# Kernel tuning notes

Hardware: AMD Instinct MI355X
Metric: run time of the kernel (lower is better)

## Reference

```python
import jax, jax.numpy as jnp
import numpy as np

EMBED_DIM = 1024
NUM_HEADS = 16
HEAD_DIM = EMBED_DIM // NUM_HEADS


def setup_inputs() -> dict:
    key = jax.random.key(0)
    k_x, k_wqkv, k_bqkv, k_wo, k_bo = jax.random.split(key, 5)
    b, n = 2, 2048
    scale_in = 1.0 / np.sqrt(EMBED_DIM)
    return {
        "x": jax.random.normal(k_x, (b, n, EMBED_DIM), dtype=jnp.float32),
        "W_qkv": jax.random.normal(k_wqkv, (EMBED_DIM, 3 * EMBED_DIM), dtype=jnp.float32) * scale_in,
        "b_qkv": jnp.zeros((3 * EMBED_DIM,), dtype=jnp.float32),
        "W_out": jax.random.normal(k_wo, (EMBED_DIM, EMBED_DIM), dtype=jnp.float32) * scale_in,
        "b_out": jnp.zeros((EMBED_DIM,), dtype=jnp.float32),
    }


def _rope_rotate(t, cos, sin):
    # t: [b, h, n, hd]; cos/sin: [1, 1, n, hd//2]
    t1, t2 = jnp.split(t, 2, axis=-1)
    return jnp.concatenate([cos * t1 - sin * t2, sin * t1 + cos * t2], axis=-1)


def reference(x, W_qkv, b_qkv, W_out, b_out):
    b, n, d = x.shape
    h, hd = NUM_HEADS, HEAD_DIM

    qkv = x @ W_qkv + b_qkv                      # [b, n, 3d]
    q, k, v = jnp.split(qkv, 3, axis=-1)
    q, k, v = [t.reshape(b, n, h, hd).transpose(0, 2, 1, 3) for t in (q, k, v)]

    # RoPE tables
    hd2 = hd // 2
    theta = 10000.0 ** (-2.0 * jnp.arange(hd2, dtype=jnp.float32) / hd)
    freqs = jnp.arange(n, dtype=jnp.float32)[:, None] * theta[None, :]  # [n, hd2]
    cos = jnp.cos(freqs)[None, None]
    sin = jnp.sin(freqs)[None, None]
    q = _rope_rotate(q, cos, sin)
    k = _rope_rotate(k, cos, sin)

    scores = jnp.einsum('bhqd,bhkd->bhqk', q, k) / jnp.sqrt(jnp.float32(hd))
    attn = jax.nn.softmax(scores, axis=-1)       # [b, h, n, n]
    out = jnp.einsum('bhqk,bhkd->bhqd', attn, v)
    out = out.transpose(0, 2, 1, 3).reshape(b, n, d)
    return out @ W_out + b_out
```

## Files before the change

kernel.cpp:

```cpp
#include <hip/hip_runtime.h>
#include <hip/hip_bf16.h>
#include <math.h>

#define EMBED 1024
#define NHEAD 16
#define HD 64
#define BATCH 2
#define SEQ 2048
#define MTOT (BATCH * SEQ)
#define QKVN (3 * EMBED)

typedef __attribute__((ext_vector_type(8))) short short8;
typedef __attribute__((ext_vector_type(4))) float f32x4;

typedef __attribute__((address_space(1))) const unsigned int GUI;
typedef __attribute__((address_space(3))) unsigned int LUI;

__device__ __forceinline__ void gload_lds16(const void* src, void* dst) {
  __builtin_amdgcn_global_load_lds((GUI*)src, (LUI*)dst, 16, 0, 0);
}

__device__ __forceinline__ unsigned short f2bf(float f) {
  unsigned u = __builtin_bit_cast(unsigned, f);
  u += 0x7fffu + ((u >> 16) & 1u);
  return (unsigned short)(u >> 16);
}

__device__ __forceinline__ unsigned cvt_pk_bf16(float lo, float hi) {
  unsigned r;
  asm("v_cvt_pk_bf16_f32 %0, %1, %2" : "=v"(r) : "v"(lo), "v"(hi));
  return r;
}

#define QSCALE 0.1803368801111191f


__global__ __launch_bounds__(256) void k_cvt(const float* __restrict__ in,
                                             unsigned short* __restrict__ out, int n4) {
  int i = blockIdx.x * 256 + threadIdx.x;
  if (i >= n4) return;
  float4 v = reinterpret_cast<const float4*>(in)[i];
  ushort4 o;
  o.x = f2bf(v.x); o.y = f2bf(v.y); o.z = f2bf(v.z); o.w = f2bf(v.w);
  reinterpret_cast<ushort4*>(out)[i] = o;
}

__global__ __launch_bounds__(256) void k_transpose_cvt(const float* __restrict__ W,
                                                       unsigned short* __restrict__ WT,
                                                       int K, int Ncols) {
  __shared__ float tile[32][33];
  int n0 = blockIdx.x * 32, k0 = blockIdx.y * 32;
  int tc = threadIdx.x & 31, tr = threadIdx.x >> 5;
  for (int i = 0; i < 4; i++) {
    int r = tr + i * 8;
    tile[r][tc] = W[(size_t)(k0 + r) * Ncols + n0 + tc];
  }
  __syncthreads();
  for (int i = 0; i < 4; i++) {
    int r = tr + i * 8;
    WT[(size_t)(n0 + r) * K + k0 + tc] = f2bf(tile[tc][r]);
  }
}

__global__ __launch_bounds__(256) void k_rope_tables(float* __restrict__ cosT,
                                                     float* __restrict__ sinT) {
  int idx = blockIdx.x * 256 + threadIdx.x;
  if (idx >= SEQ * 32) return;
  int pos = idx >> 5, i = idx & 31;
  float theta = __expf((float)i * -0.28782313662425575f);
  float f = (float)pos * theta;
  cosT[idx] = cosf(f);
  sinT[idx] = sinf(f);
}

__device__ __forceinline__ void gemm_mainloop(const unsigned short* __restrict__ A,
                                              const unsigned short* __restrict__ Bt,
                                              unsigned short* Al, unsigned short* Bl,
                                              size_t m0, size_t n0,
                                              int tid, int l15, int g, int wm, int wn,
                                              f32x4 acc[4][4]) {
  const int w = tid >> 6;
  const int lane = tid & 63;
  const int srow = lane >> 3, slot = lane & 7;
  for (int k0 = 0; k0 < 1024; k0 += 64) {
    __syncthreads();
    for (int it = 0; it < 4; it++) {
      const int r = w * 32 + it * 8 + srow;
      const int sc = (slot ^ (r & 7)) * 8;
      gload_lds16(A + (m0 + r) * 1024 + k0 + sc, &Al[(w * 32 + it * 8) * 64]);
      gload_lds16(Bt + (n0 + r) * 1024 + k0 + sc, &Bl[(w * 32 + it * 8) * 64]);
    }
    __syncthreads();
    for (int kk = 0; kk < 2; kk++) {
      short8 fa[4], fb[4];
      const int xr = ((kk * 4 + g) ^ (l15 & 7)) * 8;
      for (int i = 0; i < 4; i++)
        fa[i] = *reinterpret_cast<const short8*>(&Al[(wm * 64 + i * 16 + l15) * 64 + xr]);
      for (int j = 0; j < 4; j++)
        fb[j] = *reinterpret_cast<const short8*>(&Bl[(wn * 64 + j * 16 + l15) * 64 + xr]);
      for (int i = 0; i < 4; i++)
        for (int j = 0; j < 4; j++)
          acc[i][j] = __builtin_amdgcn_mfma_f32_16x16x32_bf16(fa[i], fb[j], acc[i][j], 0, 0, 0);
    }
  }
}

__global__ __launch_bounds__(256) void k_qkv_gemm(const unsigned short* __restrict__ A,
                                                  const unsigned short* __restrict__ Bt,
                                                  const float* __restrict__ bias,
                                                  const float* __restrict__ cosT,
                                                  const float* __restrict__ sinT,
                                                  unsigned short* __restrict__ Qb,
                                                  unsigned short* __restrict__ Kb,
                                                  unsigned short* __restrict__ Vtg) {
  __shared__ alignas(16) unsigned short Al[128 * 64];
  __shared__ alignas(16) unsigned short Bl[128 * 64];
  const int tid = threadIdx.x;
  const int lane = tid & 63, l15 = lane & 15, g = lane >> 4;
  const int wid = tid >> 6, wm = wid >> 1, wn = wid & 1;
  const size_t m0 = (size_t)blockIdx.y * 128;
  const size_t n0 = (size_t)blockIdx.x * 128;
  f32x4 acc[4][4] = {};
  gemm_mainloop(A, Bt, Al, Bl, m0, n0, tid, l15, g, wm, wn, acc);

  const int cbase = (int)n0 + wn * 64;
  const int sec = cbase >> 10;
  const int head = (cbase & 1023) >> 6;
  float bia[4];
  for (int j = 0; j < 4; j++) bia[j] = bias[cbase + j * 16 + l15];
  const size_t mw = m0 + wm * 64;

  if (sec == 2) {
    for (int i = 0; i < 4; i++) {
      size_t mbase = mw + i * 16 + g * 4;
      int bb = (int)(mbase >> 11), pos0 = (int)(mbase & 2047);
      int k0 = pos0 & 63;
      int col = (pos0 & ~63) | (k0 & 32) | (((k0 >> 2) & 3) << 3) | (((k0 >> 4) & 1) << 2);
      size_t hb = (size_t)(bb * NHEAD + head) * HD;
      for (int j = 0; j < 4; j++) {
        int d = j * 16 + l15;
        uint2 pk;
        pk.x = cvt_pk_bf16(acc[i][j][0] + bia[j], acc[i][j][1] + bia[j]);
        pk.y = cvt_pk_bf16(acc[i][j][2] + bia[j], acc[i][j][3] + bia[j]);
        *reinterpret_cast<uint2*>(Vtg + (hb + d) * SEQ + col) = pk;
      }
    }
  } else {
    unsigned short* dst = sec ? Kb : Qb;
    const float qs = sec ? 1.0f : QSCALE;
    for (int i = 0; i < 4; i++)
      for (int r = 0; r < 4; r++) {
        size_t m = mw + i * 16 + g * 4 + r;
        int bb = (int)(m >> 11), pos = (int)(m & 2047);
        size_t base = ((size_t)(bb * NHEAD + head) * SEQ + pos) * HD;
        const float* cr = cosT + pos * 32;
        const float* sr = sinT + pos * 32;
        for (int pl = 0; pl < 2; pl++) {
          int ii = pl * 16 + l15;
          float c = cr[ii], s = sr[ii];
          float lo = acc[i][pl][r] + bia[pl];
          float hi = acc[i][pl + 2][r] + bia[pl + 2];
          dst[base + ii]      = f2bf((c * lo - s * hi) * qs);
          dst[base + 32 + ii] = f2bf((s * lo + c * hi) * qs);
        }
      }
  }
}

__global__ __launch_bounds__(256) void k_out_gemm(const unsigned short* __restrict__ A,
                                                  const unsigned short* __restrict__ Bt,
                                                  const float* __restrict__ bias,
                                                  float* __restrict__ out) {
  __shared__ alignas(16) unsigned short Al[128 * 64];
  __shared__ alignas(16) unsigned short Bl[64 * 64];
  const int tid = threadIdx.x;
  const int lane = tid & 63, l15 = lane & 15, g = lane >> 4;
  const int wid = tid >> 6, wm = wid >> 1, wn = wid & 1;
  const int w = wid;
  const int srow = lane >> 3, slot = lane & 7;
  const size_t m0 = (size_t)blockIdx.y * 128;
  const size_t n0 = (size_t)blockIdx.x * 64;
  f32x4 acc[4][2] = {};

  for (int k0 = 0; k0 < 1024; k0 += 64) {
    __syncthreads();
    for (int it = 0; it < 4; it++) {
      const int r = w * 32 + it * 8 + srow;
      const int sc = (slot ^ (r & 7)) * 8;
      gload_lds16(A + (m0 + r) * 1024 + k0 + sc, &Al[(w * 32 + it * 8) * 64]);
    }
    for (int it = 0; it < 2; it++) {
      const int r = w * 16 + it * 8 + srow;
      const int sc = (slot ^ (r & 7)) * 8;
      gload_lds16(Bt + (n0 + r) * 1024 + k0 + sc, &Bl[(w * 16 + it * 8) * 64]);
    }
    __syncthreads();
    for (int kk = 0; kk < 2; kk++) {
      short8 fa[4], fb[2];
      const int xr = ((kk * 4 + g) ^ (l15 & 7)) * 8;
      for (int i = 0; i < 4; i++)
        fa[i] = *reinterpret_cast<const short8*>(&Al[(wm * 64 + i * 16 + l15) * 64 + xr]);
      for (int j = 0; j < 2; j++)
        fb[j] = *reinterpret_cast<const short8*>(&Bl[(wn * 32 + j * 16 + l15) * 64 + xr]);
      for (int i = 0; i < 4; i++)
        for (int j = 0; j < 2; j++)
          acc[i][j] = __builtin_amdgcn_mfma_f32_16x16x32_bf16(fa[i], fb[j], acc[i][j], 0, 0, 0);
    }
  }

  const int cbase = (int)n0 + wn * 32;
  const size_t mw = m0 + wm * 64;
  for (int i = 0; i < 4; i++)
    for (int r = 0; r < 4; r++) {
      size_t m = mw + i * 16 + g * 4 + r;
      for (int j = 0; j < 2; j++) {
        int col = cbase + j * 16 + l15;
        out[m * EMBED + col] = acc[i][j][r] + bias[col];
      }
    }
}

__global__ __launch_bounds__(256) void k_attn(const unsigned short* __restrict__ Q,
                                              const unsigned short* __restrict__ Kg,
                                              const unsigned short* __restrict__ Vtg,
                                              float* __restrict__ Opart,
                                              float* __restrict__ lpart) {
  __shared__ alignas(16) unsigned short Kt[64 * 64];
  __shared__ alignas(16) unsigned short Vt[64 * 64];
  const int tid = threadIdx.x, w = tid >> 6, lane = tid & 63;
  const int l15 = lane & 15, g = lane >> 4;
  const int srow = lane >> 3, slot = lane & 7;

  const int n = blockIdx.x;
  const int xcd = n & 7, m = n >> 3;
  const int qb = m & 15, z = m >> 4;
  const int sp = z & 1, bh = (z >> 1) * 8 + xcd;

  const unsigned short* Qp = Q + (size_t)bh * SEQ * HD;
  const unsigned short* Kp = Kg + (size_t)bh * SEQ * HD;
  const unsigned short* Vp = Vtg + (size_t)bh * HD * SEQ;
  const int q0 = qb * 128 + w * 32;

  short8 aq[2][2];
#pragma unroll
  for (int u = 0; u < 2; u++)
#pragma unroll
    for (int kk = 0; kk < 2; kk++)
      aq[u][kk] = *reinterpret_cast<const short8*>(
          Qp + (size_t)(q0 + u * 16 + l15) * HD + kk * 32 + g * 8);

  const int sr16 = w * 16 + srow;
  const int sc0 = (slot ^ (sr16 & 7)) * 8;

  f32x4 o[2][4] = {};
  float lrow[2] = {0.f, 0.f};

  for (int t = sp * 16; t < sp * 16 + 16; t++) {
    const int kb = t * 64;
    __syncthreads();
    gload_lds16(Kp + (size_t)(kb + sr16) * HD + sc0, &Kt[(w * 16) * 64]);
    gload_lds16(Vp + (size_t)sr16 * SEQ + kb + sc0, &Vt[(w * 16) * 64]);
    gload_lds16(Kp + (size_t)(kb + sr16 + 8) * HD + sc0, &Kt[(w * 16 + 8) * 64]);
    gload_lds16(Vp + (size_t)(sr16 + 8) * SEQ + kb + sc0, &Vt[(w * 16 + 8) * 64]);
    __syncthreads();

    f32x4 s[2][4] = {};
#pragma unroll
    for (int kk = 0; kk < 2; kk++) {
      const int xr = ((kk * 4 + g) ^ (l15 & 7)) * 8;
#pragma unroll
      for (int c = 0; c < 4; c++) {
        short8 ak = *reinterpret_cast<const short8*>(&Kt[(c * 16 + l15) * 64 + xr]);
        s[0][c] = __builtin_amdgcn_mfma_f32_16x16x32_bf16(ak, aq[0][kk], s[0][c], 0, 0, 0);
        s[1][c] = __builtin_amdgcn_mfma_f32_16x16x32_bf16(ak, aq[1][kk], s[1][c], 0, 0, 0);
      }
    }

    unsigned wpk[2][8];
#pragma unroll
    for (int u = 0; u < 2; u++) {
      float rs = 0.f;
#pragma unroll
      for (int c = 0; c < 4; c++) {
        float p0 = __builtin_exp2f(s[u][c][0]);
        float p1 = __builtin_exp2f(s[u][c][1]);
        float p2 = __builtin_exp2f(s[u][c][2]);
        float p3 = __builtin_exp2f(s[u][c][3]);
        rs += (p0 + p1) + (p2 + p3);
        wpk[u][2 * c]     = cvt_pk_bf16(p0, p1);
        wpk[u][2 * c + 1] = cvt_pk_bf16(p2, p3);
      }
      lrow[u] += rs;
    }

#pragma unroll
    for (int kk = 0; kk < 2; kk++) {
      const int xr = ((kk * 4 + g) ^ (l15 & 7)) * 8;
      short8 pb0 = __builtin_bit_cast(short8,
          uint4{wpk[0][4 * kk], wpk[0][4 * kk + 1], wpk[0][4 * kk + 2], wpk[0][4 * kk + 3]});
      short8 pb1 = __builtin_bit_cast(short8,
          uint4{wpk[1][4 * kk], wpk[1][4 * kk + 1], wpk[1][4 * kk + 2], wpk[1][4 * kk + 3]});
#pragma unroll
      for (int c2 = 0; c2 < 4; c2++) {
        short8 av = *reinterpret_cast<const short8*>(&Vt[(c2 * 16 + l15) * 64 + xr]);
        o[0][c2] = __builtin_amdgcn_mfma_f32_16x16x32_bf16(av, pb0, o[0][c2], 0, 0, 0);
        o[1][c2] = __builtin_amdgcn_mfma_f32_16x16x32_bf16(av, pb1, o[1][c2], 0, 0, 0);
      }
    }
  }

  const size_t ob = (size_t)(sp * 32 + bh) * HD * SEQ;
#pragma unroll
  for (int u = 0; u < 2; u++) {
    float l = lrow[u];
    l += __shfl_xor(l, 16, 64);
    l += __shfl_xor(l, 32, 64);
    const int pos = q0 + u * 16 + l15;
    if (g == 0) lpart[(size_t)(sp * 32 + bh) * SEQ + pos] = l;
#pragma unroll
    for (int c2 = 0; c2 < 4; c2++)
#pragma unroll
      for (int r = 0; r < 4; r++)
        Opart[ob + (size_t)(c2 * 16 + g * 4 + r) * SEQ + pos] = o[u][c2][r];
  }
}

__global__ __launch_bounds__(256) void k_merge(const float* __restrict__ Op,
                                               const float* __restrict__ lp,
                                               unsigned short* __restrict__ AO) {
  __shared__ float T[64][65];
  __shared__ float Ls[64];
  const int tid = threadIdx.x;
  const int bh = blockIdx.x & 31, pt = blockIdx.x >> 5;
  const int p0 = pt * 64;
  const size_t b0 = (size_t)bh * HD * SEQ;
  const size_t b1 = (size_t)(32 + bh) * HD * SEQ;
  const int pc = tid & 63, dr = tid >> 6;
#pragma unroll
  for (int pass = 0; pass < 16; pass++) {
    const int d = pass * 4 + dr;
    T[d][pc] = Op[b0 + (size_t)d * SEQ + p0 + pc] + Op[b1 + (size_t)d * SEQ + p0 + pc];
  }
  if (tid < 64)
    Ls[tid] = lp[(size_t)bh * SEQ + p0 + tid] + lp[(size_t)(32 + bh) * SEQ + p0 + tid];
  __syncthreads();
  const int pos = tid >> 2, dc = (tid & 3) * 16;
  const float inv = 1.f / Ls[pos];
  const int bb = bh >> 4, h = bh & 15;
  unsigned short* dst = AO + ((size_t)bb * SEQ + p0 + pos) * EMBED + h * HD + dc;
  unsigned pk[8];
#pragma unroll
  for (int i = 0; i < 8; i++)
    pk[i] = cvt_pk_bf16(T[dc + 2 * i][pos] * inv, T[dc + 2 * i + 1][pos] * inv);
  *reinterpret_cast<uint4*>(dst) = uint4{pk[0], pk[1], pk[2], pk[3]};
  *reinterpret_cast<uint4*>(dst + 8) = uint4{pk[4], pk[5], pk[6], pk[7]};
}

extern "C" void kernel_launch(void* const* d_in, const int* in_sizes, int n_in,
                              void* d_out, int out_size, void* d_ws, size_t ws_size,
                              hipStream_t stream) {
  const float* x    = (const float*)d_in[0];
  const float* Wqkv = (const float*)d_in[1];
  const float* bqkv = (const float*)d_in[2];
  const float* Wout = (const float*)d_in[3];
  const float* bout = (const float*)d_in[4];
  float* out = (float*)d_out;

  char* ws = (char*)d_ws;
  size_t off = 0;
  auto carve = [&](size_t bytes) {
    char* p = ws + off;
    off += (bytes + 255) & ~(size_t)255;
    return p;
  };
  float* cosT           = (float*)carve((size_t)SEQ * 32 * 4);
  float* sinT           = (float*)carve((size_t)SEQ * 32 * 4);
  unsigned short* Xb    = (unsigned short*)carve((size_t)MTOT * EMBED * 2);
  unsigned short* WqkvT = (unsigned short*)carve((size_t)QKVN * EMBED * 2);
  unsigned short* WoT   = (unsigned short*)carve((size_t)EMBED * EMBED * 2);
  unsigned short* Qb    = (unsigned short*)carve((size_t)MTOT * EMBED * 2);
  unsigned short* Kb    = (unsigned short*)carve((size_t)MTOT * EMBED * 2);
  unsigned short* Vtg   = (unsigned short*)carve((size_t)MTOT * EMBED * 2);
  unsigned short* AO    = (unsigned short*)carve((size_t)MTOT * EMBED * 2);
  float* Opart          = (float*)carve((size_t)2 * 32 * HD * SEQ * 4);
  float* lpart          = (float*)carve((size_t)2 * 32 * SEQ * 4);

  k_cvt<<<(MTOT * EMBED / 4 + 255) / 256, 256, 0, stream>>>(x, Xb, MTOT * EMBED / 4);
  k_transpose_cvt<<<dim3(QKVN / 32, EMBED / 32), 256, 0, stream>>>(Wqkv, WqkvT, EMBED, QKVN);
  k_transpose_cvt<<<dim3(EMBED / 32, EMBED / 32), 256, 0, stream>>>(Wout, WoT, EMBED, EMBED);
  k_rope_tables<<<(SEQ * 32) / 256, 256, 0, stream>>>(cosT, sinT);

  k_qkv_gemm<<<dim3(QKVN / 128, MTOT / 128), 256, 0, stream>>>(Xb, WqkvT, bqkv, cosT, sinT, Qb, Kb, Vtg);
  k_attn<<<dim3(1024), 256, 0, stream>>>(Qb, Kb, Vtg, Opart, lpart);
  k_merge<<<dim3(1024), 256, 0, stream>>>(Opart, lpart, AO);
  k_out_gemm<<<dim3(EMBED / 64, MTOT / 128), 256, 0, stream>>>(AO, WoT, bout, out);
}
```

Baseline: 149.4 us.

## Double-buffer K/V tiles in attention kernel to overlap loads with MFMA

Splits the K and V shared-memory tiles into two buffers. The next tile's global-to-LDS loads are issued before computing on the current one, with a partial vmcnt wait and raw barriers replacing the load-then-sync pattern. This is meant to hide global memory latency behind the QK/PV matrix work. LDS usage doubles, which could reduce occupancy.

New measurement: 146.7 us. About the same (-1.8%).

```diff
diff --git a/kernel.cpp b/kernel.cpp
--- a/kernel.cpp
+++ b/kernel.cpp
@@ -225,8 +225,8 @@
                                               const unsigned short* __restrict__ Vtg,
                                               float* __restrict__ Opart,
                                               float* __restrict__ lpart) {
-  __shared__ alignas(16) unsigned short Kt[64 * 64];
-  __shared__ alignas(16) unsigned short Vt[64 * 64];
+  __shared__ alignas(16) unsigned short Kt[2][64 * 64];
+  __shared__ alignas(16) unsigned short Vt[2][64 * 64];
   const int tid = threadIdx.x, w = tid >> 6, lane = tid & 63;
   const int l15 = lane & 15, g = lane >> 4;
   const int srow = lane >> 3, slot = lane & 7;
@@ -251,63 +251,79 @@
 
   const int sr16 = w * 16 + srow;
   const int sc0 = (slot ^ (sr16 & 7)) * 8;
+  const int kb0 = sp * 1024;
 
   f32x4 o[2][4] = {};
   float lrow[2] = {0.f, 0.f};
 
-  for (int t = sp * 16; t < sp * 16 + 16; t++) {
-    const int kb = t * 64;
-    __syncthreads();
-    gload_lds16(Kp + (size_t)(kb + sr16) * HD + sc0, &Kt[(w * 16) * 64]);
-    gload_lds16(Vp + (size_t)sr16 * SEQ + kb + sc0, &Vt[(w * 16) * 64]);
-    gload_lds16(Kp + (size_t)(kb + sr16 + 8) * HD + sc0, &Kt[(w * 16 + 8) * 64]);
-    gload_lds16(Vp + (size_t)(sr16 + 8) * SEQ + kb + sc0, &Vt[(w * 16 + 8) * 64]);
-    __syncthreads();
-
-    f32x4 s[2][4] = {};
-#pragma unroll
-    for (int kk = 0; kk < 2; kk++) {
-      const int xr = ((kk * 4 + g) ^ (l15 & 7)) * 8;
-#pragma unroll
-      for (int c = 0; c < 4; c++) {
-        short8 ak = *reinterpret_cast<const short8*>(&Kt[(c * 16 + l15) * 64 + xr]);
-        s[0][c] = __builtin_amdgcn_mfma_f32_16x16x32_bf16(ak, aq[0][kk], s[0][c], 0, 0, 0);
-        s[1][c] = __builtin_amdgcn_mfma_f32_16x16x32_bf16(ak, aq[1][kk], s[1][c], 0, 0, 0);
-      }
-    }
-
-    unsigned wpk[2][8];
-#pragma unroll
-    for (int u = 0; u < 2; u++) {
-      float rs = 0.f;
-#pragma unroll
-      for (int c = 0; c < 4; c++) {
-        float p0 = __builtin_exp2f(s[u][c][0]);
-        float p1 = __builtin_exp2f(s[u][c][1]);
-        float p2 = __builtin_exp2f(s[u][c][2]);
-        float p3 = __builtin_exp2f(s[u][c][3]);
-        rs += (p0 + p1) + (p2 + p3);
-        wpk[u][2 * c]     = cvt_pk_bf16(p0, p1);
-        wpk[u][2 * c + 1] = cvt_pk_bf16(p2, p3);
-      }
-      lrow[u] += rs;
-    }
-
-#pragma unroll
-    for (int kk = 0; kk < 2; kk++) {
-      const int xr = ((kk * 4 + g) ^ (l15 & 7)) * 8;
-      short8 pb0 = __builtin_bit_cast(short8,
-          uint4{wpk[0][4 * kk], wpk[0][4 * kk + 1], wpk[0][4 * kk + 2], wpk[0][4 * kk + 3]});
-      short8 pb1 = __builtin_bit_cast(short8,
-          uint4{wpk[1][4 * kk], wpk[1][4 * kk + 1], wpk[1][4 * kk + 2], wpk[1][4 * kk + 3]});
-#pragma unroll
-      for (int c2 = 0; c2 < 4; c2++) {
-        short8 av = *reinterpret_cast<const short8*>(&Vt[(c2 * 16 + l15) * 64 + xr]);
-        o[0][c2] = __builtin_amdgcn_mfma_f32_16x16x32_bf16(av, pb0, o[0][c2], 0, 0, 0);
-        o[1][c2] = __builtin_amdgcn_mfma_f32_16x16x32_bf16(av, pb1, o[1][c2], 0, 0, 0);
-      }
-    }
-  }
+#define STAGE(tt, b)                                                             \
+  do {                                                                           \
+    const int kb_ = kb0 + (tt) * 64;                                             \
+    gload_lds16(Kp + (size_t)(kb_ + sr16) * HD + sc0, &Kt[b][(w * 16) * 64]);    \
+    gload_lds16(Vp + (size_t)sr16 * SEQ + kb_ + sc0, &Vt[b][(w * 16) * 64]);     \
+    gload_lds16(Kp + (size_t)(kb_ + sr16 + 8) * HD + sc0,                        \
+                &Kt[b][(w * 16 + 8) * 64]);                                      \
+    gload_lds16(Vp + (size_t)(sr16 + 8) * SEQ + kb_ + sc0,                       \
+                &Vt[b][(w * 16 + 8) * 64]);                                      \
+  } while (0)
+
+#define COMPUTE(cur)                                                             \
+  do {                                                                           \
+    const unsigned short* Ktc = Kt[cur];                                         \
+    const unsigned short* Vtc = Vt[cur];                                         \
+    f32x4 s[2][4] = {};                                                          \
+    _Pragma("unroll") for (int kk = 0; kk < 2; kk++) {                           \
+      const int xr = ((kk * 4 + g) ^ (l15 & 7)) * 8;                             \
+      _Pragma("unroll") for (int c = 0; c < 4; c++) {                            \
+        short8 ak = *reinterpret_cast<const short8*>(&Ktc[(c * 16 + l15) * 64 + xr]); \
+        s[0][c] = __builtin_amdgcn_mfma_f32_16x16x32_bf16(ak, aq[0][kk], s[0][c], 0, 0, 0); \
+        s[1][c] = __builtin_amdgcn_mfma_f32_16x16x32_bf16(ak, aq[1][kk], s[1][c], 0, 0, 0); \
+      }                                                                          \
+    }                                                                            \
+    unsigned wpk[2][8];                                                          \
+    _Pragma("unroll") for (int u = 0; u < 2; u++) {                              \
+      float rs = 0.f;                                                            \
+      _Pragma("unroll") for (int c = 0; c < 4; c++) {                            \
+        float p0 = __builtin_exp2f(s[u][c][0]);                                  \
+        float p1 = __builtin_exp2f(s[u][c][1]);                                  \
+        float p2 = __builtin_exp2f(s[u][c][2]);                                  \
+        float p3 = __builtin_exp2f(s[u][c][3]);                                  \
+        rs += (p0 + p1) + (p2 + p3);                                             \
+        wpk[u][2 * c]     = cvt_pk_bf16(p0, p1);                                 \
+        wpk[u][2 * c + 1] = cvt_pk_bf16(p2, p3);                                 \
+      }                                                                          \
+      lrow[u] += rs;                                                             \
+    }                                                                            \
+    _Pragma("unroll") for (int kk = 0; kk < 2; kk++) {                           \
+      const int xr = ((kk * 4 + g) ^ (l15 & 7)) * 8;                             \
+      short8 pb0 = __builtin_bit_cast(short8,                                    \
+          uint4{wpk[0][4 * kk], wpk[0][4 * kk + 1], wpk[0][4 * kk + 2], wpk[0][4 * kk + 3]}); \
+      short8 pb1 = __builtin_bit_cast(short8,                                    \
+          uint4{wpk[1][4 * kk], wpk[1][4 * kk + 1], wpk[1][4 * kk + 2], wpk[1][4 * kk + 3]}); \
+      _Pragma("unroll") for (int c2 = 0; c2 < 4; c2++) {                         \
+        short8 av = *reinterpret_cast<const short8*>(&Vtc[(c2 * 16 + l15) * 64 + xr]); \
+        o[0][c2] = __builtin_amdgcn_mfma_f32_16x16x32_bf16(av, pb0, o[0][c2], 0, 0, 0); \
+        o[1][c2] = __builtin_amdgcn_mfma_f32_16x16x32_bf16(av, pb1, o[1][c2], 0, 0, 0); \
+      }                                                                          \
+    }                                                                            \
+  } while (0)
+
+  STAGE(0, 0);
+
+  for (int t = 0; t < 15; t++) {
+    const int cur = t & 1;
+    STAGE(t + 1, cur ^ 1);
+    asm volatile("s_waitcnt vmcnt(4)" ::: "memory");
+    __builtin_amdgcn_s_barrier();
+    COMPUTE(cur);
+    __builtin_amdgcn_s_barrier();
+  }
+  asm volatile("s_waitcnt vmcnt(0)" ::: "memory");
+  __builtin_amdgcn_s_barrier();
+  COMPUTE(1);
+
+#undef STAGE
+#undef COMPUTE
 
   const size_t ob = (size_t)(sp * 32 + bh) * HD * SEQ;
 #pragma unroll
```
